# Optimization experiments

Hardware: AMD Instinct MI355X
Metric: run time of the kernel (lower is better)

The kernel has to match this reference:

```python
import jax, jax.numpy as jnp
import numpy as np

N, E, D, H, G = 50000, 1_600_000, 13, 32, 128
EPS = 1e-5


def _lin(k, fan_in, fan_out):
    kw, kb = jax.random.split(k)
    bound = 1.0 / np.sqrt(fan_in)
    W = jax.random.uniform(kw, (fan_in, fan_out), jnp.float32, -bound, bound)
    b = jax.random.uniform(kb, (fan_out,), jnp.float32, -bound, bound)
    return W, b


def setup_inputs() -> dict:
    key = jax.random.key(0)
    ks = jax.random.split(key, 10)
    x = jax.random.normal(ks[0], (N, D), jnp.float32)
    edge_index = jax.random.randint(ks[1], (2, E), 0, N)
    batch = jnp.sort(jax.random.randint(ks[2], (N,), 0, G))
    bn_gamma = jnp.ones((D,), jnp.float32)
    bn_beta = jnp.zeros((D,), jnp.float32)
    in_w1, in_b1 = _lin(ks[3], D, H)
    in_w2, in_b2 = _lin(ks[4], H, H)
    conv_w1, conv_b1 = _lin(ks[5], 2 * (H + D), 2 * H)
    conv_w2, conv_b2 = _lin(ks[6], 2 * H, H)
    out_w1, out_b1 = _lin(ks[7], H + D, H)
    out_w2, out_b2 = _lin(ks[8], H, 1)
    return dict(x=x, edge_index=edge_index, batch=batch,
                bn_gamma=bn_gamma, bn_beta=bn_beta,
                in_w1=in_w1, in_b1=in_b1, in_w2=in_w2, in_b2=in_b2,
                conv_w1=conv_w1, conv_b1=conv_b1, conv_w2=conv_w2, conv_b2=conv_b2,
                out_w1=out_w1, out_b1=out_b1, out_w2=out_w2, out_b2=out_b2)


def reference(x, edge_index, batch, bn_gamma, bn_beta,
              in_w1, in_b1, in_w2, in_b2,
              conv_w1, conv_b1, conv_w2, conv_b2,
              out_w1, out_b1, out_w2, out_b2):
    # BatchNorm1d (training-mode batch statistics, biased variance)
    mu = jnp.mean(x, axis=0)
    var = jnp.mean((x - mu) ** 2, axis=0)
    X = (x - mu) / jnp.sqrt(var + EPS) * bn_gamma + bn_beta  # [N, D]
    # inputnet
    Hn = jnp.tanh(jax.nn.relu(X @ in_w1 + in_b1) @ in_w2 + in_b2)  # [N, H]
    feat = jnp.concatenate([Hn, X], axis=-1)  # [N, H+D]
    # n_iters = 1 EdgeConv iteration: message = nn([x_i, x_j - x_i]), aggr='add' at target i
    src, dst = edge_index[0], edge_index[1]
    x_i = feat[dst]                               # [E, H+D] target
    x_j = feat[src]                               # [E, H+D] source
    m = jnp.concatenate([x_i, x_j - x_i], axis=-1)  # [E, 2(H+D)]
    m = jnp.tanh(jax.nn.relu(m @ conv_w1 + conv_b1) @ conv_w2 + conv_b2)  # [E, H]
    Hn = jax.ops.segment_sum(m, dst, num_segments=N)  # [N, H]
    feat = jnp.concatenate([Hn, X], axis=-1)  # [N, H+D]
    # global_mean_pool over graphs
    sums = jax.ops.segment_sum(feat, batch, num_segments=G)  # [G, H+D]
    counts = jax.ops.segment_sum(jnp.ones((feat.shape[0], 1), feat.dtype), batch, num_segments=G)
    x_mean = sums / jnp.maximum(counts, 1.0)
    # outputnet
    return jax.nn.sigmoid(jax.nn.relu(x_mean @ out_w1 + out_b1) @ out_w2 + out_b2)  # [G, 1]
```

## Files before the change

kernel.cpp:

```cpp
#include <hip/hip_runtime.h>


typedef __attribute__((ext_vector_type(4))) float floatx4;
typedef __attribute__((ext_vector_type(8))) short short8;
typedef __attribute__((ext_vector_type(8))) _Float16 half8;
typedef __attribute__((ext_vector_type(2))) __fp16 fp16x2;

__device__ __forceinline__ unsigned short f2bf(float f) {
    unsigned int u = __float_as_uint(f);
    u += 0x7FFFu + ((u >> 16) & 1u);
    return (unsigned short)(u >> 16);
}
__device__ __forceinline__ unsigned short f2h(float f) {
    _Float16 h = (_Float16)f;
    return __builtin_bit_cast(unsigned short, h);
}
__device__ __forceinline__ float h2f(unsigned short u) {
    return (float)__builtin_bit_cast(_Float16, u);
}
__device__ __forceinline__ float fast_tanh(float x) {
    float ax = fminf(fabsf(x), 20.0f);
    float e = __expf(2.0f * ax);
    float r = 1.0f - 2.0f * __builtin_amdgcn_rcpf(e + 1.0f);
    return copysignf(r, x);
}
__device__ __forceinline__ float fast_sigmoid(float x) {
    float xc = fminf(fmaxf(x, -30.f), 30.f);
    return 1.0f / (1.0f + __expf(-xc));
}
__device__ __forceinline__ unsigned int pk_h2(float a, float b) {
    fp16x2 p = __builtin_amdgcn_cvt_pkrtz(a, b);
    return __builtin_bit_cast(unsigned int, p);
}
__device__ __forceinline__ void atomic_pk_add_f16(unsigned short* addr, unsigned int packed) {
    asm volatile("global_atomic_pk_add_f16 %0, %1, off" :: "v"(addr), "v"(packed) : "memory");
}

#define NBLK_STAT 120

__global__ __launch_bounds__(256) void k_bnstat(const float* __restrict__ x, int N,
                                                float* __restrict__ part,
                                                uint4* __restrict__ HnZ, int hnq,
                                                float* __restrict__ gacc, int gn) {
    int tid = blockIdx.x * blockDim.x + threadIdx.x;
    int stride = gridDim.x * blockDim.x;
    uint4 z4 = make_uint4(0u, 0u, 0u, 0u);
    for (int i = tid; i < hnq; i += stride) HnZ[i] = z4;
    for (int i = tid; i < gn; i += stride) gacc[i] = 0.f;

    float s[13], q[13];
#pragma unroll
    for (int d = 0; d < 13; d++) { s[d] = 0.f; q[d] = 0.f; }
    for (int n = tid; n < N; n += stride) {
        const float* row = x + (size_t)n * 13;
#pragma unroll
        for (int d = 0; d < 13; d++) { float f = row[d]; s[d] += f; q[d] += f * f; }
    }
#pragma unroll
    for (int d = 0; d < 13; d++) {
        for (int off = 32; off > 0; off >>= 1) {
            s[d] += __shfl_down(s[d], off, 64);
            q[d] += __shfl_down(q[d], off, 64);
        }
    }
    __shared__ float red[4][26];
    int w = threadIdx.x >> 6;
    if ((threadIdx.x & 63) == 0) {
#pragma unroll
        for (int d = 0; d < 13; d++) { red[w][d] = s[d]; red[w][13 + d] = q[d]; }
    }
    __syncthreads();
    if (threadIdx.x < 26) {
        float v = red[0][threadIdx.x] + red[1][threadIdx.x] + red[2][threadIdx.x] + red[3][threadIdx.x];
        int d = threadIdx.x;
        if (d < 13) part[blockIdx.x * 32 + d] = v;
        else        part[NBLK_STAT * 32 + blockIdx.x * 32 + (d - 13)] = v;
    }
}

#define FP 72
#define WP 72
__global__ __launch_bounds__(128) void k_node(
    const float* __restrict__ x, const int* __restrict__ batch,
    const float* __restrict__ bn_g, const float* __restrict__ bn_b,
    const float* __restrict__ in_w1, const float* __restrict__ in_b1,
    const float* __restrict__ in_w2, const float* __restrict__ in_b2,
    const float* __restrict__ conv_w1, const float* __restrict__ conv_b1,
    const float* __restrict__ part,
    unsigned short* __restrict__ A, unsigned short* __restrict__ Bm,
    float* __restrict__ gacc, int N) {
    __shared__ float sW1[13 * 32], sB1[32], sW2[32 * 32], sB2[32];
    __shared__ float sScl[16], sShf[16];
    __shared__ unsigned short sWcatT[128 * WP];
    __shared__ unsigned short sFeat[128 * FP];
    int tid = threadIdx.x;

    for (int i = tid; i < 13 * 32; i += 128) sW1[i] = in_w1[i];
    if (tid < 32) { sB1[tid] = in_b1[tid]; sB2[tid] = in_b2[tid]; }
    for (int i = tid; i < 32 * 32; i += 128) sW2[i] = in_w2[i];
    for (int i = tid; i < 128 * 64; i += 128) {
        int c = i >> 6, k = i & 63;
        float v = 0.f;
        if (k < 45) {
            int cc = c & 63;
            float bot = conv_w1[(45 + k) * 64 + cc];
            v = (c < 64) ? (conv_w1[k * 64 + cc] - bot) : bot;
        }
        sWcatT[c * WP + k] = f2bf(v);
    }
    if (tid < 13) {
        float su = 0.f, sq = 0.f;
        for (int b = 0; b < NBLK_STAT; b++) {
            su += part[b * 32 + tid];
            sq += part[NBLK_STAT * 32 + b * 32 + tid];
        }
        float invN = 1.0f / (float)N;
        float mu = su * invN;
        float var = fmaxf(sq * invN - mu * mu, 0.f);
        float sc = bn_g[tid] / sqrtf(var + 1e-5f);
        sScl[tid] = sc;
        sShf[tid] = bn_b[tid] - mu * sc;
    }
    __syncthreads();

    int n = blockIdx.x * 128 + tid;
    bool valid = (n < N);
    int nl = valid ? n : (N - 1);

    float X[13];
#pragma unroll
    for (int d = 0; d < 13; d++)
        X[d] = x[(size_t)nl * 13 + d] * sScl[d] + sShf[d];
    float h1[32];
#pragma unroll
    for (int j = 0; j < 32; j++) {
        float acc = sB1[j];
#pragma unroll
        for (int d = 0; d < 13; d++) acc += X[d] * sW1[d * 32 + j];
        h1[j] = fmaxf(acc, 0.f);
    }
    float h2[32];
#pragma unroll
    for (int j = 0; j < 32; j++) {
        float acc = sB2[j];
#pragma unroll
        for (int k = 0; k < 32; k++) acc += h1[k] * sW2[k * 32 + j];
        h2[j] = fast_tanh(acc);
    }

    unsigned int fw[16];
#pragma unroll
    for (int i = 0; i < 16; i++) fw[i] = 0;
    if (valid) {
#pragma unroll
        for (int i = 0; i < 16; i++)
            fw[i] = (unsigned)f2bf(h2[2 * i]) | ((unsigned)f2bf(h2[2 * i + 1]) << 16);
    }
    unsigned int xw[7];
#pragma unroll
    for (int i = 0; i < 7; i++) xw[i] = 0;
    if (valid) {
#pragma unroll
        for (int i = 0; i < 6; i++)
            xw[i] = (unsigned)f2bf(X[2 * i]) | ((unsigned)f2bf(X[2 * i + 1]) << 16);
        xw[6] = (unsigned)f2bf(X[12]);
    }
    {
        unsigned short* row = sFeat + tid * FP;
        ((uint4*)row)[0] = make_uint4(fw[0], fw[1], fw[2], fw[3]);
        ((uint4*)row)[1] = make_uint4(fw[4], fw[5], fw[6], fw[7]);
        ((uint4*)row)[2] = make_uint4(fw[8], fw[9], fw[10], fw[11]);
        ((uint4*)row)[3] = make_uint4(fw[12], fw[13], fw[14], fw[15]);
        ((uint4*)row)[4] = make_uint4(xw[0], xw[1], xw[2], xw[3]);
        ((uint4*)row)[5] = make_uint4(xw[4], xw[5], xw[6], 0u);
        ((uint4*)row)[6] = make_uint4(0u, 0u, 0u, 0u);
        ((uint4*)row)[7] = make_uint4(0u, 0u, 0u, 0u);
    }

    {
        int g = valid ? batch[n] : -1;
        unsigned long long uni = __ballot(g == __shfl(g, 0, 64));
        if (uni == ~0ull && g >= 0) {
            float red[14];
#pragma unroll
            for (int d = 0; d < 13; d++) red[d] = X[d];
            red[13] = 1.0f;
#pragma unroll
            for (int d = 0; d < 14; d++)
                for (int off = 32; off > 0; off >>= 1)
                    red[d] += __shfl_down(red[d], off, 64);
            if ((tid & 63) == 0) {
#pragma unroll
                for (int d = 0; d < 13; d++) unsafeAtomicAdd(&gacc[g * 46 + 32 + d], red[d]);
                unsafeAtomicAdd(&gacc[g * 46 + 45], red[13]);
            }
        } else if (valid) {
#pragma unroll
            for (int d = 0; d < 13; d++) unsafeAtomicAdd(&gacc[g * 46 + 32 + d], X[d]);
            unsafeAtomicAdd(&gacc[g * 46 + 45], 1.0f);
        }
    }
    __syncthreads();

    int lane = tid & 63;
    int w = tid >> 6;
    int q = lane >> 4;
    int m = lane & 15;

    short8 wf[2][8];
#pragma unroll
    for (int ks = 0; ks < 2; ks++)
#pragma unroll
        for (int t = 0; t < 8; t++) {
            wf[ks][t] = *(const short8*)(sWcatT + (t * 16 + m) * WP + ks * 32 + q * 8);
        }
    float cb1v[4];
#pragma unroll
    for (int t = 0; t < 4; t++) cb1v[t] = conv_b1[t * 16 + m];

    int base = blockIdx.x * 128 + w * 64;
#pragma unroll
    for (int tile = 0; tile < 4; tile++) {
        const unsigned short* ar = sFeat + (w * 64 + tile * 16 + m) * FP;
        short8 a0 = *(const short8*)(ar + q * 8);
        short8 a1 = *(const short8*)(ar + 32 + q * 8);
        floatx4 c[8];
#pragma unroll
        for (int t = 0; t < 8; t++) {
            floatx4 z = {0.f, 0.f, 0.f, 0.f};
            c[t] = __builtin_amdgcn_mfma_f32_16x16x32_bf16(a0, wf[0][t], z, 0, 0, 0);
            c[t] = __builtin_amdgcn_mfma_f32_16x16x32_bf16(a1, wf[1][t], c[t], 0, 0, 0);
        }
#pragma unroll
        for (int r = 0; r < 4; r++) {
            int row = base + tile * 16 + (q << 2) + r;
            if (row < N) {
#pragma unroll
                for (int t = 0; t < 4; t++)
                    A[(size_t)row * 64 + t * 16 + m] = f2h(c[t][r] + cb1v[t]);
#pragma unroll
                for (int t = 4; t < 8; t++)
                    Bm[(size_t)row * 64 + (t - 4) * 16 + m] = f2h(c[t][r]);
            }
        }
    }
}

__global__ __launch_bounds__(256) void k_edge(
    const int* __restrict__ ei,
    const unsigned short* __restrict__ A, const unsigned short* __restrict__ Bm,
    const float* __restrict__ conv_w2, const float* __restrict__ conv_b2,
    unsigned short* __restrict__ Hn, int E) {
    int lane = threadIdx.x & 63;
    int wid  = blockIdx.x * (blockDim.x >> 6) + (threadIdx.x >> 6);
    int nw   = gridDim.x * (blockDim.x >> 6);
    int q = lane >> 4;
    int m = lane & 15;

    half8 wf[2][2];
#pragma unroll
    for (int s = 0; s < 2; s++)
#pragma unroll
        for (int t = 0; t < 2; t++)
#pragma unroll
            for (int j = 0; j < 8; j++)
                wf[s][t][j] = (_Float16)conv_w2[(s * 32 + q * 8 + j) * 32 + 2 * m + t];
    float cb2a = conv_b2[2 * m];
    float cb2b = conv_b2[2 * m + 1];

    const int* srcp = ei;
    const int* dstp = ei + E;
    int npairs = E >> 5;

    const half8 zero8 = (half8)(_Float16)0.0f;

    for (int p = wid; p < npairs; p += nw) {
        int e0 = p << 5;
        int vd0 = dstp[e0 + m];
        int vs0 = srcp[e0 + m];
        int vd1 = dstp[e0 + 16 + m];
        int vs1 = srcp[e0 + 16 + m];
        uint4 av0a = *(const uint4*)(A  + (size_t)vd0 * 64 + q * 8);
        uint4 av0b = *(const uint4*)(A  + (size_t)vd0 * 64 + 32 + q * 8);
        uint4 bv0a = *(const uint4*)(Bm + (size_t)vs0 * 64 + q * 8);
        uint4 bv0b = *(const uint4*)(Bm + (size_t)vs0 * 64 + 32 + q * 8);
        uint4 av1a = *(const uint4*)(A  + (size_t)vd1 * 64 + q * 8);
        uint4 av1b = *(const uint4*)(A  + (size_t)vd1 * 64 + 32 + q * 8);
        uint4 bv1a = *(const uint4*)(Bm + (size_t)vs1 * 64 + q * 8);
        uint4 bv1b = *(const uint4*)(Bm + (size_t)vs1 * 64 + 32 + q * 8);

        floatx4 c00 = {0.f, 0.f, 0.f, 0.f}, c01 = {0.f, 0.f, 0.f, 0.f};
        floatx4 c10 = {0.f, 0.f, 0.f, 0.f}, c11 = {0.f, 0.f, 0.f, 0.f};

        auto mk = [&zero8](uint4 av, uint4 bv) -> half8 {
            half8 a = __builtin_bit_cast(half8, av);
            half8 b = __builtin_bit_cast(half8, bv);
            half8 s = a + b;
            return __builtin_elementwise_max(s, zero8);
        };
        half8 h0a = mk(av0a, bv0a);
        half8 h0b = mk(av0b, bv0b);
        half8 h1a = mk(av1a, bv1a);
        half8 h1b = mk(av1b, bv1b);

        c00 = __builtin_amdgcn_mfma_f32_16x16x32_f16(h0a, wf[0][0], c00, 0, 0, 0);
        c01 = __builtin_amdgcn_mfma_f32_16x16x32_f16(h0a, wf[0][1], c01, 0, 0, 0);
        c10 = __builtin_amdgcn_mfma_f32_16x16x32_f16(h1a, wf[0][0], c10, 0, 0, 0);
        c11 = __builtin_amdgcn_mfma_f32_16x16x32_f16(h1a, wf[0][1], c11, 0, 0, 0);
        c00 = __builtin_amdgcn_mfma_f32_16x16x32_f16(h0b, wf[1][0], c00, 0, 0, 0);
        c01 = __builtin_amdgcn_mfma_f32_16x16x32_f16(h0b, wf[1][1], c01, 0, 0, 0);
        c10 = __builtin_amdgcn_mfma_f32_16x16x32_f16(h1b, wf[1][0], c10, 0, 0, 0);
        c11 = __builtin_amdgcn_mfma_f32_16x16x32_f16(h1b, wf[1][1], c11, 0, 0, 0);

#pragma unroll
        for (int r = 0; r < 4; r++) {
            int m2 = (q << 2) + r;
            int dd0 = __shfl(vd0, m2, 64);
            int dd1 = __shfl(vd1, m2, 64);
            float o00 = fast_tanh(c00[r] + cb2a);
            float o01 = fast_tanh(c01[r] + cb2b);
            float o10 = fast_tanh(c10[r] + cb2a);
            float o11 = fast_tanh(c11[r] + cb2b);
            atomic_pk_add_f16(Hn + (size_t)dd0 * 32 + 2 * m, pk_h2(o00, o01));
            atomic_pk_add_f16(Hn + (size_t)dd1 * 32 + 2 * m, pk_h2(o10, o11));
        }
    }

    int tstart = npairs << 5;
    int tail = E - tstart;
    if (tail && wid == 0 && lane < tail) {
        int e = tstart + lane;
        int vd = dstp[e], vs = srcp[e];
        float h[64];
        for (int k = 0; k < 64; k++) {
            float a = h2f(A[(size_t)vd * 64 + k]);
            float b = h2f(Bm[(size_t)vs * 64 + k]);
            h[k] = fmaxf(a + b, 0.f);
        }
        for (int j = 0; j < 16; j++) {
            float acc0 = conv_b2[2 * j], acc1 = conv_b2[2 * j + 1];
            for (int k = 0; k < 64; k++) {
                acc0 += h[k] * conv_w2[k * 32 + 2 * j];
                acc1 += h[k] * conv_w2[k * 32 + 2 * j + 1];
            }
            atomic_pk_add_f16(Hn + (size_t)vd * 32 + 2 * j, pk_h2(fast_tanh(acc0), fast_tanh(acc1)));
        }
    }
}

__global__ __launch_bounds__(256) void k_pool(const unsigned short* __restrict__ Hn,
                                              const int* __restrict__ batch,
                                              float* __restrict__ gacc, int N) {
    const int NPB = 512;
    int c = threadIdx.x & 31;
    int r = threadIdx.x >> 5;
    int n0 = blockIdx.x * NPB;
    int nend = min(n0 + NPB, N);
    int gcur = -1;
    float acc = 0.f;
    for (int n = n0 + r; n < nend; n += 8) {
        int g = batch[n];
        if (g != gcur) {
            if (gcur >= 0) unsafeAtomicAdd(&gacc[gcur * 46 + c], acc);
            gcur = g; acc = 0.f;
        }
        acc += h2f(Hn[(size_t)n * 32 + c]);
    }
    if (gcur >= 0) unsafeAtomicAdd(&gacc[gcur * 46 + c], acc);
}

__global__ void k_out(const float* __restrict__ gacc,
                      const float* __restrict__ out_w1, const float* __restrict__ out_b1,
                      const float* __restrict__ out_w2, const float* __restrict__ out_b2,
                      float* __restrict__ out, int G) {
    int g = blockIdx.x * blockDim.x + threadIdx.x;
    if (g >= G) return;
    float cnt = fmaxf(gacc[g * 46 + 45], 1.0f);
    float inv = 1.0f / cnt;
    float f[45];
#pragma unroll
    for (int i = 0; i < 45; i++) f[i] = gacc[g * 46 + i] * inv;
    float h[32];
#pragma unroll
    for (int j = 0; j < 32; j++) {
        float acc = out_b1[j];
#pragma unroll
        for (int k = 0; k < 45; k++) acc += f[k] * out_w1[k * 32 + j];
        h[j] = fmaxf(acc, 0.f);
    }
    float o = out_b2[0];
#pragma unroll
    for (int j = 0; j < 32; j++) o += h[j] * out_w2[j];
    out[g] = fast_sigmoid(o);
}

extern "C" void kernel_launch(void* const* d_in, const int* in_sizes, int n_in,
                              void* d_out, int out_size, void* d_ws, size_t ws_size,
                              hipStream_t stream) {
    const float* x      = (const float*)d_in[0];
    const int*   ei     = (const int*)d_in[1];
    const int*   batch  = (const int*)d_in[2];
    const float* bn_g   = (const float*)d_in[3];
    const float* bn_b   = (const float*)d_in[4];
    const float* in_w1  = (const float*)d_in[5];
    const float* in_b1  = (const float*)d_in[6];
    const float* in_w2  = (const float*)d_in[7];
    const float* in_b2  = (const float*)d_in[8];
    const float* cw1    = (const float*)d_in[9];
    const float* cb1    = (const float*)d_in[10];
    const float* cw2    = (const float*)d_in[11];
    const float* cb2    = (const float*)d_in[12];
    const float* ow1    = (const float*)d_in[13];
    const float* ob1    = (const float*)d_in[14];
    const float* ow2    = (const float*)d_in[15];
    const float* ob2    = (const float*)d_in[16];

    int N = in_sizes[0] / 13;
    int E = in_sizes[1] / 2;
    int G = out_size;
    int Npad = (N + 255) & ~255;

    auto al = [](size_t v) { return (v + 255) & ~(size_t)255; };
    char* ws = (char*)d_ws;
    size_t hn_off   = 0;
    size_t gacc_off = al((size_t)N * 32 * 2);
    size_t part_off = gacc_off + al((size_t)G * 46 * 4);
    size_t a_off    = part_off + al(2 * NBLK_STAT * 32 * 4);
    size_t b_off    = a_off + al((size_t)Npad * 64 * 2);

    unsigned short* Hn = (unsigned short*)(ws + hn_off);
    float* gacc = (float*)(ws + gacc_off);
    float* part = (float*)(ws + part_off);
    unsigned short* A  = (unsigned short*)(ws + a_off);
    unsigned short* Bm = (unsigned short*)(ws + b_off);

    int hnq = (N * 32 * 2) / 16;
    int gn  = G * 46;

    k_bnstat<<<NBLK_STAT, 256, 0, stream>>>(x, N, part, (uint4*)Hn, hnq, gacc, gn);
    k_node<<<(N + 127) / 128, 128, 0, stream>>>(x, batch, bn_g, bn_b,
                                                in_w1, in_b1, in_w2, in_b2,
                                                cw1, cb1, part, A, Bm, gacc, N);
    k_edge<<<2048, 256, 0, stream>>>(ei, A, Bm, cw2, cb2, Hn, E);
    k_pool<<<(N + 511) / 512, 256, 0, stream>>>(Hn, batch, gacc, N);
    k_out<<<1, 128, 0, stream>>>(gacc, ow1, ob1, ow2, ob2, (float*)d_out, G);
}
```

Baseline: 285.9 us.

## Bucket edges by destination and aggregate in shared memory instead of global atomics

Adds a counting sort of edges into destination-node buckets of 128 nodes: count, scan, then scatter packed source and local-destination pairs. Each bucket is then processed by one block that accumulates messages in fp32 shared memory and writes Hn once, replacing the fp16 global packed atomics and the Hn zeroing. The intent is to remove global atomic contention and gain locality on destination rows. The cost is three extra kernels that each read the edge list, and the 16-bit source packing assumes N < 65536. It also parallelises the BatchNorm partial reduction in k_node.

```diff
diff --git a/kernel.cpp b/kernel.cpp
--- a/kernel.cpp
+++ b/kernel.cpp
@@ -32,21 +32,20 @@
     fp16x2 p = __builtin_amdgcn_cvt_pkrtz(a, b);
     return __builtin_bit_cast(unsigned int, p);
 }
-__device__ __forceinline__ void atomic_pk_add_f16(unsigned short* addr, unsigned int packed) {
-    asm volatile("global_atomic_pk_add_f16 %0, %1, off" :: "v"(addr), "v"(packed) : "memory");
-}
 
 #define NBLK_STAT 120
+#define BKT_BITS 7
+#define BKT_SZ 128
+#define NPART 256
 
 __global__ __launch_bounds__(256) void k_bnstat(const float* __restrict__ x, int N,
                                                 float* __restrict__ part,
-                                                uint4* __restrict__ HnZ, int hnq,
-                                                float* __restrict__ gacc, int gn) {
+                                                float* __restrict__ gacc, int gn,
+                                                int* __restrict__ bt, int nb) {
     int tid = blockIdx.x * blockDim.x + threadIdx.x;
     int stride = gridDim.x * blockDim.x;
-    uint4 z4 = make_uint4(0u, 0u, 0u, 0u);
-    for (int i = tid; i < hnq; i += stride) HnZ[i] = z4;
     for (int i = tid; i < gn; i += stride) gacc[i] = 0.f;
+    for (int i = tid; i < nb; i += stride) bt[i] = 0;
 
     float s[13], q[13];
 #pragma unroll
@@ -75,6 +74,66 @@
         int d = threadIdx.x;
         if (d < 13) part[blockIdx.x * 32 + d] = v;
         else        part[NBLK_STAT * 32 + blockIdx.x * 32 + (d - 13)] = v;
+    }
+}
+
+__global__ __launch_bounds__(256) void k_count(const int* __restrict__ ei, int E, int CH,
+                                               int* __restrict__ bt, int nb) {
+    __shared__ int h[512];
+    const int* dstp = ei + E;
+    int tid = threadIdx.x;
+    for (int i = tid; i < nb; i += 256) h[i] = 0;
+    __syncthreads();
+    int e0 = blockIdx.x * CH;
+    int e1 = min(e0 + CH, E);
+    for (int e = e0 + tid; e < e1; e += 256)
+        atomicAdd(&h[dstp[e] >> BKT_BITS], 1);
+    __syncthreads();
+    for (int i = tid; i < nb; i += 256)
+        if (h[i] > 0) atomicAdd(&bt[i], h[i]);
+}
+
+__global__ __launch_bounds__(512) void k_scanB(const int* __restrict__ bt,
+                                               int* __restrict__ base,
+                                               int* __restrict__ gcur, int nb, int E) {
+    __shared__ int sd[512];
+    int t = threadIdx.x;
+    int v = (t < nb) ? bt[t] : 0;
+    sd[t] = v;
+    __syncthreads();
+    for (int off = 1; off < 512; off <<= 1) {
+        int a = (t >= off) ? sd[t - off] : 0;
+        __syncthreads();
+        sd[t] += a;
+        __syncthreads();
+    }
+    int excl = sd[t] - v;
+    if (t < nb) { base[t] = excl; gcur[t] = excl; }
+    if (t == 0) base[nb] = E;
+}
+
+__global__ __launch_bounds__(256) void k_scat(const int* __restrict__ ei, int E, int CH,
+                                              int* __restrict__ gcur,
+                                              unsigned* __restrict__ packed, int nb) {
+    __shared__ int h[512], cur[512];
+    const int* srcp = ei;
+    const int* dstp = ei + E;
+    int tid = threadIdx.x;
+    for (int i = tid; i < nb; i += 256) h[i] = 0;
+    __syncthreads();
+    int e0 = blockIdx.x * CH;
+    int e1 = min(e0 + CH, E);
+    for (int e = e0 + tid; e < e1; e += 256)
+        atomicAdd(&h[dstp[e] >> BKT_BITS], 1);
+    __syncthreads();
+    for (int i = tid; i < nb; i += 256)
+        cur[i] = (h[i] > 0) ? atomicAdd(&gcur[i], h[i]) : 0;
+    __syncthreads();
+    for (int e = e0 + tid; e < e1; e += 256) {
+        int d = dstp[e];
+        int b = d >> BKT_BITS;
+        int pos = atomicAdd(&cur[b], 1);
+        packed[pos] = (unsigned)srcp[e] | ((unsigned)(d & (BKT_SZ - 1)) << 16);
     }
 }
 
@@ -91,6 +150,7 @@
     float* __restrict__ gacc, int N) {
     __shared__ float sW1[13 * 32], sB1[32], sW2[32 * 32], sB2[32];
     __shared__ float sScl[16], sShf[16];
+    __shared__ float sRedS[13][8], sRedQ[13][8];
     __shared__ unsigned short sWcatT[128 * WP];
     __shared__ unsigned short sFeat[128 * FP];
     int tid = threadIdx.x;
@@ -108,12 +168,20 @@
         }
         sWcatT[c * WP + k] = f2bf(v);
     }
+    if (tid < 104) {
+        int d = tid >> 3, j = tid & 7;
+        float su = 0.f, sq = 0.f;
+        for (int b = j; b < NBLK_STAT; b += 8) {
+            su += part[b * 32 + d];
+            sq += part[NBLK_STAT * 32 + b * 32 + d];
+        }
+        sRedS[d][j] = su; sRedQ[d][j] = sq;
+    }
+    __syncthreads();
     if (tid < 13) {
         float su = 0.f, sq = 0.f;
-        for (int b = 0; b < NBLK_STAT; b++) {
-            su += part[b * 32 + tid];
-            sq += part[NBLK_STAT * 32 + b * 32 + tid];
-        }
+#pragma unroll
+        for (int j = 0; j < 8; j++) { su += sRedS[tid][j]; sq += sRedQ[tid][j]; }
         float invN = 1.0f / (float)N;
         float mu = su * invN;
         float var = fmaxf(sq * invN - mu * mu, 0.f);
@@ -246,14 +314,22 @@
     }
 }
 
-__global__ __launch_bounds__(256) void k_edge(
-    const int* __restrict__ ei,
+__global__ __launch_bounds__(256) void k_agg(
+    const unsigned* __restrict__ packed, const int* __restrict__ base,
     const unsigned short* __restrict__ A, const unsigned short* __restrict__ Bm,
     const float* __restrict__ conv_w2, const float* __restrict__ conv_b2,
-    unsigned short* __restrict__ Hn, int E) {
-    int lane = threadIdx.x & 63;
-    int wid  = blockIdx.x * (blockDim.x >> 6) + (threadIdx.x >> 6);
-    int nw   = gridDim.x * (blockDim.x >> 6);
+    unsigned short* __restrict__ Hn, int N) {
+    __shared__ float sAcc[BKT_SZ][32];
+    int tid = threadIdx.x;
+    for (int i = tid; i < BKT_SZ * 32; i += 256) ((float*)sAcc)[i] = 0.f;
+
+    int bucket = blockIdx.x;
+    int n0 = bucket << BKT_BITS;
+    int beg = base[bucket], end = base[bucket + 1];
+    int cnt = end - beg;
+
+    int lane = tid & 63;
+    int w = tid >> 6;
     int q = lane >> 4;
     int m = lane & 15;
 
@@ -267,84 +343,54 @@
                 wf[s][t][j] = (_Float16)conv_w2[(s * 32 + q * 8 + j) * 32 + 2 * m + t];
     float cb2a = conv_b2[2 * m];
     float cb2b = conv_b2[2 * m + 1];
-
-    const int* srcp = ei;
-    const int* dstp = ei + E;
-    int npairs = E >> 5;
-
     const half8 zero8 = (half8)(_Float16)0.0f;
 
-    for (int p = wid; p < npairs; p += nw) {
-        int e0 = p << 5;
-        int vd0 = dstp[e0 + m];
-        int vs0 = srcp[e0 + m];
-        int vd1 = dstp[e0 + 16 + m];
-        int vs1 = srcp[e0 + 16 + m];
-        uint4 av0a = *(const uint4*)(A  + (size_t)vd0 * 64 + q * 8);
-        uint4 av0b = *(const uint4*)(A  + (size_t)vd0 * 64 + 32 + q * 8);
-        uint4 bv0a = *(const uint4*)(Bm + (size_t)vs0 * 64 + q * 8);
-        uint4 bv0b = *(const uint4*)(Bm + (size_t)vs0 * 64 + 32 + q * 8);
-        uint4 av1a = *(const uint4*)(A  + (size_t)vd1 * 64 + q * 8);
-        uint4 av1b = *(const uint4*)(A  + (size_t)vd1 * 64 + 32 + q * 8);
-        uint4 bv1a = *(const uint4*)(Bm + (size_t)vs1 * 64 + q * 8);
-        uint4 bv1b = *(const uint4*)(Bm + (size_t)vs1 * 64 + 32 + q * 8);
-
-        floatx4 c00 = {0.f, 0.f, 0.f, 0.f}, c01 = {0.f, 0.f, 0.f, 0.f};
-        floatx4 c10 = {0.f, 0.f, 0.f, 0.f}, c11 = {0.f, 0.f, 0.f, 0.f};
-
-        auto mk = [&zero8](uint4 av, uint4 bv) -> half8 {
-            half8 a = __builtin_bit_cast(half8, av);
-            half8 b = __builtin_bit_cast(half8, bv);
-            half8 s = a + b;
-            return __builtin_elementwise_max(s, zero8);
-        };
-        half8 h0a = mk(av0a, bv0a);
-        half8 h0b = mk(av0b, bv0b);
-        half8 h1a = mk(av1a, bv1a);
-        half8 h1b = mk(av1b, bv1b);
-
-        c00 = __builtin_amdgcn_mfma_f32_16x16x32_f16(h0a, wf[0][0], c00, 0, 0, 0);
-        c01 = __builtin_amdgcn_mfma_f32_16x16x32_f16(h0a, wf[0][1], c01, 0, 0, 0);
-        c10 = __builtin_amdgcn_mfma_f32_16x16x32_f16(h1a, wf[0][0], c10, 0, 0, 0);
-        c11 = __builtin_amdgcn_mfma_f32_16x16x32_f16(h1a, wf[0][1], c11, 0, 0, 0);
-        c00 = __builtin_amdgcn_mfma_f32_16x16x32_f16(h0b, wf[1][0], c00, 0, 0, 0);
-        c01 = __builtin_amdgcn_mfma_f32_16x16x32_f16(h0b, wf[1][1], c01, 0, 0, 0);
-        c10 = __builtin_amdgcn_mfma_f32_16x16x32_f16(h1b, wf[1][0], c10, 0, 0, 0);
-        c11 = __builtin_amdgcn_mfma_f32_16x16x32_f16(h1b, wf[1][1], c11, 0, 0, 0);
+    __syncthreads();
+
+    int ngrp = (cnt + 15) >> 4;
+    for (int g = w; g < ngrp; g += 4) {
+        int o = beg + (g << 4);
+        unsigned pk = packed[min(o + m, end - 1)];
+        int src = (int)(pk & 0xFFFFu);
+        int dlo = (int)((pk >> 16) & (BKT_SZ - 1));
+        size_t drow = (size_t)(n0 + dlo) * 64;
+        uint4 ava = *(const uint4*)(A + drow + q * 8);
+        uint4 avb = *(const uint4*)(A + drow + 32 + q * 8);
+        uint4 bva = *(const uint4*)(Bm + (size_t)src * 64 + q * 8);
+        uint4 bvb = *(const uint4*)(Bm + (size_t)src * 64 + 32 + q * 8);
+
+        half8 ha = __builtin_elementwise_max(
+            __builtin_bit_cast(half8, ava) + __builtin_bit_cast(half8, bva), zero8);
+        half8 hb = __builtin_elementwise_max(
+            __builtin_bit_cast(half8, avb) + __builtin_bit_cast(half8, bvb), zero8);
+
+        floatx4 c0 = {0.f, 0.f, 0.f, 0.f}, c1 = {0.f, 0.f, 0.f, 0.f};
+        c0 = __builtin_amdgcn_mfma_f32_16x16x32_f16(ha, wf[0][0], c0, 0, 0, 0);
+        c1 = __builtin_amdgcn_mfma_f32_16x16x32_f16(ha, wf[0][1], c1, 0, 0, 0);
+        c0 = __builtin_amdgcn_mfma_f32_16x16x32_f16(hb, wf[1][0], c0, 0, 0, 0);
+        c1 = __builtin_amdgcn_mfma_f32_16x16x32_f16(hb, wf[1][1], c1, 0, 0, 0);
 
 #pragma unroll
         for (int r = 0; r < 4; r++) {
-            int m2 = (q << 2) + r;
-            int dd0 = __shfl(vd0, m2, 64);
-            int dd1 = __shfl(vd1, m2, 64);
-            float o00 = fast_tanh(c00[r] + cb2a);
-            float o01 = fast_tanh(c01[r] + cb2b);
-            float o10 = fast_tanh(c10[r] + cb2a);
-            float o11 = fast_tanh(c11[r] + cb2b);
-            atomic_pk_add_f16(Hn + (size_t)dd0 * 32 + 2 * m, pk_h2(o00, o01));
-            atomic_pk_add_f16(Hn + (size_t)dd1 * 32 + 2 * m, pk_h2(o10, o11));
-        }
-    }
-
-    int tstart = npairs << 5;
-    int tail = E - tstart;
-    if (tail && wid == 0 && lane < tail) {
-        int e = tstart + lane;
-        int vd = dstp[e], vs = srcp[e];
-        float h[64];
-        for (int k = 0; k < 64; k++) {
-            float a = h2f(A[(size_t)vd * 64 + k]);
-            float b = h2f(Bm[(size_t)vs * 64 + k]);
-            h[k] = fmaxf(a + b, 0.f);
-        }
-        for (int j = 0; j < 16; j++) {
-            float acc0 = conv_b2[2 * j], acc1 = conv_b2[2 * j + 1];
-            for (int k = 0; k < 64; k++) {
-                acc0 += h[k] * conv_w2[k * 32 + 2 * j];
-                acc1 += h[k] * conv_w2[k * 32 + 2 * j + 1];
+            int eg = (q << 2) + r;
+            int dloe = __shfl(dlo, eg, 64);
+            bool valid = ((g << 4) + eg) < cnt;
+            float t0 = fast_tanh(c0[r] + cb2a);
+            float t1 = fast_tanh(c1[r] + cb2b);
+            if (valid) {
+                atomicAdd(&sAcc[dloe][2 * m], t0);
+                atomicAdd(&sAcc[dloe][2 * m + 1], t1);
             }
-            atomic_pk_add_f16(Hn + (size_t)vd * 32 + 2 * j, pk_h2(fast_tanh(acc0), fast_tanh(acc1)));
-        }
+        }
+    }
+    __syncthreads();
+
+    for (int i = tid; i < BKT_SZ * 16; i += 256) {
+        int row = i >> 4, c2 = i & 15;
+        int n = n0 + row;
+        if (n < N)
+            *(unsigned*)(Hn + (size_t)n * 32 + 2 * c2) =
+                pk_h2(sAcc[row][2 * c2], sAcc[row][2 * c2 + 1]);
     }
 }
 
@@ -419,6 +465,8 @@
     int E = in_sizes[1] / 2;
     int G = out_size;
     int Npad = (N + 255) & ~255;
+    int NB = (N + BKT_SZ - 1) >> BKT_BITS;
+    int CH = (E + NPART - 1) / NPART;
 
     auto al = [](size_t v) { return (v + 255) & ~(size_t)255; };
     char* ws = (char*)d_ws;
@@ -427,21 +475,31 @@
     size_t part_off = gacc_off + al((size_t)G * 46 * 4);
     size_t a_off    = part_off + al(2 * NBLK_STAT * 32 * 4);
     size_t b_off    = a_off + al((size_t)Npad * 64 * 2);
+    size_t bt_off   = b_off + al((size_t)Npad * 64 * 2);
+    size_t base_off = bt_off + al((size_t)(NB + 1) * 4);
+    size_t gcur_off = base_off + al((size_t)(NB + 1) * 4);
+    size_t pk_off   = gcur_off + al((size_t)(NB + 1) * 4);
 
     unsigned short* Hn = (unsigned short*)(ws + hn_off);
     float* gacc = (float*)(ws + gacc_off);
     float* part = (float*)(ws + part_off);
     unsigned short* A  = (unsigned short*)(ws + a_off);
     unsigned short* Bm = (unsigned short*)(ws + b_off);
-
-    int hnq = (N * 32 * 2) / 16;
-    int gn  = G * 46;
-
-    k_bnstat<<<NBLK_STAT, 256, 0, stream>>>(x, N, part, (uint4*)Hn, hnq, gacc, gn);
+    int* bt     = (int*)(ws + bt_off);
+    int* baseA  = (int*)(ws + base_off);
+    int* gcur   = (int*)(ws + gcur_off);
+    unsigned* packed = (unsigned*)(ws + pk_off);
+
+    int gn = G * 46;
+
+    k_bnstat<<<NBLK_STAT, 256, 0, stream>>>(x, N, part, gacc, gn, bt, NB);
+    k_count<<<NPART, 256, 0, stream>>>(ei, E, CH, bt, NB);
+    k_scanB<<<1, 512, 0, stream>>>(bt, baseA, gcur, NB, E);
+    k_scat<<<NPART, 256, 0, stream>>>(ei, E, CH, gcur, packed, NB);
     k_node<<<(N + 127) / 128, 128, 0, stream>>>(x, batch, bn_g, bn_b,
                                                 in_w1, in_b1, in_w2, in_b2,
                                                 cw1, cb1, part, A, Bm, gacc, N);
-    k_edge<<<2048, 256, 0, stream>>>(ei, A, Bm, cw2, cb2, Hn, E);
+    k_agg<<<NB, 256, 0, stream>>>(packed, baseA, A, Bm, cw2, cb2, Hn, N);
     k_pool<<<(N + 511) / 512, 256, 0, stream>>>(Hn, batch, gacc, N);
     k_out<<<1, 128, 0, stream>>>(gacc, ow1, ob1, ow2, ob2, (float*)d_out, G);
 }
```

After: 587.5 us. 2.05x slower.

## Split node kernel into MLP and GEMM stages, precompute conv weights once

Applied to the files above, without the earlier changes.

Moves the per-block conv_w1 transform and bf16 conversion into the stats kernel, so it runs once into a workspace buffer instead of once per block. The node kernel is split: k_nodeA runs the input MLP with 256-thread blocks and writes bf16 features to global memory, and k_nodeB does the MFMA projection to A/Bm with 64 rows per block. The BN partial-sum reduction is parallelised across 104 threads, and k_pool uses smaller chunks for more blocks. In exchange it adds an extra kernel launch and a global round trip for the feature buffer.

```diff
diff --git a/kernel.cpp b/kernel.cpp
--- a/kernel.cpp
+++ b/kernel.cpp
@@ -41,12 +41,24 @@
 __global__ __launch_bounds__(256) void k_bnstat(const float* __restrict__ x, int N,
                                                 float* __restrict__ part,
                                                 uint4* __restrict__ HnZ, int hnq,
-                                                float* __restrict__ gacc, int gn) {
+                                                float* __restrict__ gacc, int gn,
+                                                const float* __restrict__ conv_w1,
+                                                unsigned short* __restrict__ wcat) {
     int tid = blockIdx.x * blockDim.x + threadIdx.x;
     int stride = gridDim.x * blockDim.x;
     uint4 z4 = make_uint4(0u, 0u, 0u, 0u);
     for (int i = tid; i < hnq; i += stride) HnZ[i] = z4;
     for (int i = tid; i < gn; i += stride) gacc[i] = 0.f;
+    for (int i = tid; i < 128 * 64; i += stride) {
+        int c = i >> 6, k = i & 63;
+        float v = 0.f;
+        if (k < 45) {
+            int cc = c & 63;
+            float bot = conv_w1[(45 + k) * 64 + cc];
+            v = (c < 64) ? (conv_w1[k * 64 + cc] - bot) : bot;
+        }
+        wcat[i] = f2bf(v);
+    }
 
     float s[13], q[13];
 #pragma unroll
@@ -78,42 +90,36 @@
     }
 }
 
-#define FP 72
-#define WP 72
-__global__ __launch_bounds__(128) void k_node(
+__global__ __launch_bounds__(256) void k_nodeA(
     const float* __restrict__ x, const int* __restrict__ batch,
     const float* __restrict__ bn_g, const float* __restrict__ bn_b,
     const float* __restrict__ in_w1, const float* __restrict__ in_b1,
     const float* __restrict__ in_w2, const float* __restrict__ in_b2,
-    const float* __restrict__ conv_w1, const float* __restrict__ conv_b1,
     const float* __restrict__ part,
-    unsigned short* __restrict__ A, unsigned short* __restrict__ Bm,
-    float* __restrict__ gacc, int N) {
+    unsigned short* __restrict__ feat, float* __restrict__ gacc, int N) {
     __shared__ float sW1[13 * 32], sB1[32], sW2[32 * 32], sB2[32];
     __shared__ float sScl[16], sShf[16];
-    __shared__ unsigned short sWcatT[128 * WP];
-    __shared__ unsigned short sFeat[128 * FP];
+    __shared__ float sRedS[13][8], sRedQ[13][8];
+    __shared__ unsigned short sFeat[256 * 64];
     int tid = threadIdx.x;
 
-    for (int i = tid; i < 13 * 32; i += 128) sW1[i] = in_w1[i];
+    for (int i = tid; i < 13 * 32; i += 256) sW1[i] = in_w1[i];
     if (tid < 32) { sB1[tid] = in_b1[tid]; sB2[tid] = in_b2[tid]; }
-    for (int i = tid; i < 32 * 32; i += 128) sW2[i] = in_w2[i];
-    for (int i = tid; i < 128 * 64; i += 128) {
-        int c = i >> 6, k = i & 63;
-        float v = 0.f;
-        if (k < 45) {
-            int cc = c & 63;
-            float bot = conv_w1[(45 + k) * 64 + cc];
-            v = (c < 64) ? (conv_w1[k * 64 + cc] - bot) : bot;
-        }
-        sWcatT[c * WP + k] = f2bf(v);
-    }
+    for (int i = tid; i < 32 * 32; i += 256) sW2[i] = in_w2[i];
+    if (tid < 104) {
+        int d = tid >> 3, j = tid & 7;
+        float su = 0.f, sq = 0.f;
+        for (int b = j; b < NBLK_STAT; b += 8) {
+            su += part[b * 32 + d];
+            sq += part[NBLK_STAT * 32 + b * 32 + d];
+        }
+        sRedS[d][j] = su; sRedQ[d][j] = sq;
+    }
+    __syncthreads();
     if (tid < 13) {
         float su = 0.f, sq = 0.f;
-        for (int b = 0; b < NBLK_STAT; b++) {
-            su += part[b * 32 + tid];
-            sq += part[NBLK_STAT * 32 + b * 32 + tid];
-        }
+#pragma unroll
+        for (int j = 0; j < 8; j++) { su += sRedS[tid][j]; sq += sRedQ[tid][j]; }
         float invN = 1.0f / (float)N;
         float mu = su * invN;
         float var = fmaxf(sq * invN - mu * mu, 0.f);
@@ -123,7 +129,7 @@
     }
     __syncthreads();
 
-    int n = blockIdx.x * 128 + tid;
+    int n = blockIdx.x * 256 + tid;
     bool valid = (n < N);
     int nl = valid ? n : (N - 1);
 
@@ -151,22 +157,20 @@
     unsigned int fw[16];
 #pragma unroll
     for (int i = 0; i < 16; i++) fw[i] = 0;
+    unsigned int xw[7];
+#pragma unroll
+    for (int i = 0; i < 7; i++) xw[i] = 0;
     if (valid) {
 #pragma unroll
         for (int i = 0; i < 16; i++)
             fw[i] = (unsigned)f2bf(h2[2 * i]) | ((unsigned)f2bf(h2[2 * i + 1]) << 16);
-    }
-    unsigned int xw[7];
-#pragma unroll
-    for (int i = 0; i < 7; i++) xw[i] = 0;
-    if (valid) {
 #pragma unroll
         for (int i = 0; i < 6; i++)
             xw[i] = (unsigned)f2bf(X[2 * i]) | ((unsigned)f2bf(X[2 * i + 1]) << 16);
         xw[6] = (unsigned)f2bf(X[12]);
     }
     {
-        unsigned short* row = sFeat + tid * FP;
+        unsigned short* row = sFeat + tid * 64;
         ((uint4*)row)[0] = make_uint4(fw[0], fw[1], fw[2], fw[3]);
         ((uint4*)row)[1] = make_uint4(fw[4], fw[5], fw[6], fw[7]);
         ((uint4*)row)[2] = make_uint4(fw[8], fw[9], fw[10], fw[11]);
@@ -202,6 +206,17 @@
     }
     __syncthreads();
 
+    uint4* dst = (uint4*)(feat + (size_t)blockIdx.x * 256 * 64);
+    const uint4* srcq = (const uint4*)sFeat;
+#pragma unroll
+    for (int j = 0; j < 8; j++) dst[tid + j * 256] = srcq[tid + j * 256];
+}
+
+__global__ __launch_bounds__(256) void k_nodeB(
+    const unsigned short* __restrict__ feat, const unsigned short* __restrict__ wcat,
+    const float* __restrict__ conv_b1,
+    unsigned short* __restrict__ A, unsigned short* __restrict__ Bm, int N) {
+    int tid = threadIdx.x;
     int lane = tid & 63;
     int w = tid >> 6;
     int q = lane >> 4;
@@ -211,37 +226,33 @@
 #pragma unroll
     for (int ks = 0; ks < 2; ks++)
 #pragma unroll
-        for (int t = 0; t < 8; t++) {
-            wf[ks][t] = *(const short8*)(sWcatT + (t * 16 + m) * WP + ks * 32 + q * 8);
-        }
+        for (int t = 0; t < 8; t++)
+            wf[ks][t] = *(const short8*)(wcat + (t * 16 + m) * 64 + ks * 32 + q * 8);
     float cb1v[4];
 #pragma unroll
     for (int t = 0; t < 4; t++) cb1v[t] = conv_b1[t * 16 + m];
 
-    int base = blockIdx.x * 128 + w * 64;
-#pragma unroll
-    for (int tile = 0; tile < 4; tile++) {
-        const unsigned short* ar = sFeat + (w * 64 + tile * 16 + m) * FP;
-        short8 a0 = *(const short8*)(ar + q * 8);
-        short8 a1 = *(const short8*)(ar + 32 + q * 8);
-        floatx4 c[8];
-#pragma unroll
-        for (int t = 0; t < 8; t++) {
-            floatx4 z = {0.f, 0.f, 0.f, 0.f};
-            c[t] = __builtin_amdgcn_mfma_f32_16x16x32_bf16(a0, wf[0][t], z, 0, 0, 0);
-            c[t] = __builtin_amdgcn_mfma_f32_16x16x32_bf16(a1, wf[1][t], c[t], 0, 0, 0);
-        }
-#pragma unroll
-        for (int r = 0; r < 4; r++) {
-            int row = base + tile * 16 + (q << 2) + r;
-            if (row < N) {
-#pragma unroll
-                for (int t = 0; t < 4; t++)
-                    A[(size_t)row * 64 + t * 16 + m] = f2h(c[t][r] + cb1v[t]);
-#pragma unroll
-                for (int t = 4; t < 8; t++)
-                    Bm[(size_t)row * 64 + (t - 4) * 16 + m] = f2h(c[t][r]);
-            }
+    int row0 = blockIdx.x * 64 + w * 16;
+    const unsigned short* ar = feat + (size_t)(row0 + m) * 64;
+    short8 a0 = *(const short8*)(ar + q * 8);
+    short8 a1 = *(const short8*)(ar + 32 + q * 8);
+    floatx4 c[8];
+#pragma unroll
+    for (int t = 0; t < 8; t++) {
+        floatx4 z = {0.f, 0.f, 0.f, 0.f};
+        c[t] = __builtin_amdgcn_mfma_f32_16x16x32_bf16(a0, wf[0][t], z, 0, 0, 0);
+        c[t] = __builtin_amdgcn_mfma_f32_16x16x32_bf16(a1, wf[1][t], c[t], 0, 0, 0);
+    }
+#pragma unroll
+    for (int r = 0; r < 4; r++) {
+        int row = row0 + (q << 2) + r;
+        if (row < N) {
+#pragma unroll
+            for (int t = 0; t < 4; t++)
+                A[(size_t)row * 64 + t * 16 + m] = f2h(c[t][r] + cb1v[t]);
+#pragma unroll
+            for (int t = 4; t < 8; t++)
+                Bm[(size_t)row * 64 + (t - 4) * 16 + m] = f2h(c[t][r]);
         }
     }
 }
@@ -289,9 +300,6 @@
         uint4 bv1a = *(const uint4*)(Bm + (size_t)vs1 * 64 + q * 8);
         uint4 bv1b = *(const uint4*)(Bm + (size_t)vs1 * 64 + 32 + q * 8);
 
-        floatx4 c00 = {0.f, 0.f, 0.f, 0.f}, c01 = {0.f, 0.f, 0.f, 0.f};
-        floatx4 c10 = {0.f, 0.f, 0.f, 0.f}, c11 = {0.f, 0.f, 0.f, 0.f};
-
         auto mk = [&zero8](uint4 av, uint4 bv) -> half8 {
             half8 a = __builtin_bit_cast(half8, av);
             half8 b = __builtin_bit_cast(half8, bv);
@@ -303,6 +311,8 @@
         half8 h1a = mk(av1a, bv1a);
         half8 h1b = mk(av1b, bv1b);
 
+        floatx4 c00 = {0.f, 0.f, 0.f, 0.f}, c01 = {0.f, 0.f, 0.f, 0.f};
+        floatx4 c10 = {0.f, 0.f, 0.f, 0.f}, c11 = {0.f, 0.f, 0.f, 0.f};
         c00 = __builtin_amdgcn_mfma_f32_16x16x32_f16(h0a, wf[0][0], c00, 0, 0, 0);
         c01 = __builtin_amdgcn_mfma_f32_16x16x32_f16(h0a, wf[0][1], c01, 0, 0, 0);
         c10 = __builtin_amdgcn_mfma_f32_16x16x32_f16(h1a, wf[0][0], c10, 0, 0, 0);
@@ -351,7 +361,7 @@
 __global__ __launch_bounds__(256) void k_pool(const unsigned short* __restrict__ Hn,
                                               const int* __restrict__ batch,
                                               float* __restrict__ gacc, int N) {
-    const int NPB = 512;
+    const int NPB = 128;
     int c = threadIdx.x & 31;
     int r = threadIdx.x >> 5;
     int n0 = blockIdx.x * NPB;
@@ -427,21 +437,27 @@
     size_t part_off = gacc_off + al((size_t)G * 46 * 4);
     size_t a_off    = part_off + al(2 * NBLK_STAT * 32 * 4);
     size_t b_off    = a_off + al((size_t)Npad * 64 * 2);
-
-    unsigned short* Hn = (unsigned short*)(ws + hn_off);
-    float* gacc = (float*)(ws + gacc_off);
-    float* part = (float*)(ws + part_off);
-    unsigned short* A  = (unsigned short*)(ws + a_off);
-    unsigned short* Bm = (unsigned short*)(ws + b_off);
+    size_t ft_off   = b_off + al((size_t)Npad * 64 * 2);
+    size_t wc_off   = ft_off + al((size_t)Npad * 64 * 2);
+
+    unsigned short* Hn   = (unsigned short*)(ws + hn_off);
+    float* gacc          = (float*)(ws + gacc_off);
+    float* part          = (float*)(ws + part_off);
+    unsigned short* A    = (unsigned short*)(ws + a_off);
+    unsigned short* Bm   = (unsigned short*)(ws + b_off);
+    unsigned short* feat = (unsigned short*)(ws + ft_off);
+    unsigned short* wcat = (unsigned short*)(ws + wc_off);
 
     int hnq = (N * 32 * 2) / 16;
     int gn  = G * 46;
 
-    k_bnstat<<<NBLK_STAT, 256, 0, stream>>>(x, N, part, (uint4*)Hn, hnq, gacc, gn);
-    k_node<<<(N + 127) / 128, 128, 0, stream>>>(x, batch, bn_g, bn_b,
-                                                in_w1, in_b1, in_w2, in_b2,
-                                                cw1, cb1, part, A, Bm, gacc, N);
+    k_bnstat<<<NBLK_STAT, 256, 0, stream>>>(x, N, part, (uint4*)Hn, hnq, gacc, gn,
+                                            cw1, wcat);
+    k_nodeA<<<Npad / 256, 256, 0, stream>>>(x, batch, bn_g, bn_b,
+                                            in_w1, in_b1, in_w2, in_b2,
+                                            part, feat, gacc, N);
+    k_nodeB<<<Npad / 64, 256, 0, stream>>>(feat, wcat, cb1, A, Bm, N);
     k_edge<<<2048, 256, 0, stream>>>(ei, A, Bm, cw2, cb2, Hn, E);
-    k_pool<<<(N + 511) / 512, 256, 0, stream>>>(Hn, batch, gacc, N);
+    k_pool<<<(N + 127) / 128, 256, 0, stream>>>(Hn, batch, gacc, N);
     k_out<<<1, 128, 0, stream>>>(gacc, ow1, ob1, ow2, ob2, (float*)d_out, G);
 }
```

After: 261.2 us, median of 2. 1.09x faster.
